# Kernel optimization log

Hardware: AMD Instinct MI355X
Metric: run time of the kernel (lower is better)

The kernel has to match this reference:

```python
import jax, jax.numpy as jnp
import numpy as np

EMBED_DIM = 512
NUM_HEADS = 8
HEAD_DIM = EMBED_DIM // NUM_HEADS
N = 4096
E = 131072
EPS = 1e-5
NEG = -1e9


def layer_norm(x, g, b):
    mu = jnp.mean(x, axis=-1, keepdims=True)
    var = jnp.mean(jnp.square(x - mu), axis=-1, keepdims=True)
    return (x - mu) * jax.lax.rsqrt(var + EPS) * g + b


def setup_inputs() -> dict:
    key = jax.random.key(0)
    ks = jax.random.split(key, 12)
    D = EMBED_DIM
    s = 1.0 / np.sqrt(D)
    return {
        "x": jax.random.normal(ks[0], (N, D), jnp.float32),
        "edge_index": jax.random.randint(ks[1], (2, E), 0, N, jnp.int64),
        "edge_weight": jax.random.uniform(ks[2], (E,), jnp.float32),
        "Wqkv": jax.random.normal(ks[3], (3 * D, D), jnp.float32) * s,
        "bqkv": jnp.zeros((3 * D,), jnp.float32),
        "Wo": jax.random.normal(ks[4], (D, D), jnp.float32) * s,
        "bo": jnp.zeros((D,), jnp.float32),
        "W1": jax.random.normal(ks[5], (D, D), jnp.float32) * s,
        "b1": jnp.zeros((D,), jnp.float32),
        "g1": jnp.ones((D,), jnp.float32),
        "beta1": jnp.zeros((D,), jnp.float32),
        "g2": jnp.ones((D,), jnp.float32),
        "beta2": jnp.zeros((D,), jnp.float32),
    }


def reference(x, edge_index, edge_weight, Wqkv, bqkv, Wo, bo, W1, b1, g1, beta1, g2, beta2):
    n = x.shape[0]
    # dense NxN additive bias: -1e9 everywhere, 0 on diagonal, edge weights at (dst, src)
    src, dst = edge_index[0], edge_index[1]
    diag = jnp.arange(n)
    bias = jnp.full((n, n), NEG, dtype=x.dtype)
    bias = bias.at[diag, diag].set(0.0)
    bias = bias.at[dst, src].set(edge_weight.astype(x.dtype))

    # multi-head self-attention (torch nn.MultiheadAttention semantics)
    qkv = x @ Wqkv.T + bqkv                       # (N, 3D)
    q, k, v = jnp.split(qkv, 3, axis=-1)          # each (N, D)
    q = q.reshape(n, NUM_HEADS, HEAD_DIM).transpose(1, 0, 2)  # (H, N, hd)
    k = k.reshape(n, NUM_HEADS, HEAD_DIM).transpose(1, 0, 2)
    v = v.reshape(n, NUM_HEADS, HEAD_DIM).transpose(1, 0, 2)
    scores = jnp.einsum("hnd,hmd->hnm", q, k) / np.sqrt(HEAD_DIM)  # (H, N, N)
    scores = scores + bias[None, :, :]
    attn = jax.nn.softmax(scores, axis=-1)
    out = jnp.einsum("hnm,hmd->hnd", attn, v)     # (H, N, hd)
    out = out.transpose(1, 0, 2).reshape(n, EMBED_DIM)
    attn_out = out @ Wo.T + bo

    # residual + LN + FFN (single linear, no activation) + residual + LN
    h = layer_norm(x + attn_out, g1, beta1)
    h = layer_norm(h + (h @ W1.T + b1), g2, beta2)
    return h
```

## Files before the change

### kernel.cpp

```cpp
#include <hip/hip_runtime.h>

#define NNODES 4096
#define DIM 512
#define QKVD 1536
#define MAXE 96

typedef __bf16 bf16_t;
typedef bf16_t bf16x8 __attribute__((ext_vector_type(8)));
typedef bf16_t bf16x2 __attribute__((ext_vector_type(2)));
typedef float f32x4 __attribute__((ext_vector_type(4)));
typedef unsigned int uint;

__global__ __launch_bounds__(256) void cast_all_k(const float* __restrict__ x,
                                                  const float* __restrict__ wqkv,
                                                  const float* __restrict__ wo,
                                                  const float* __restrict__ w1,
                                                  bf16_t* __restrict__ xb,
                                                  bf16_t* __restrict__ wqkvb,
                                                  bf16_t* __restrict__ wob,
                                                  bf16_t* __restrict__ w1b,
                                                  uint* __restrict__ deg) {
  int i = blockIdx.x * 256 + threadIdx.x;
  if (blockIdx.x < 16) deg[i] = 0u;
  const float* src;
  bf16_t* dst;
  int off;
  if (i < 524288) { src = x; dst = xb; off = i; }
  else if (i < 720896) { src = wqkv; dst = wqkvb; off = i - 524288; }
  else if (i < 786432) { src = wo; dst = wob; off = i - 720896; }
  else { src = w1; dst = w1b; off = i - 786432; }
  float4 v = ((const float4*)src)[off];
  dst[4 * off + 0] = (bf16_t)v.x;
  dst[4 * off + 1] = (bf16_t)v.y;
  dst[4 * off + 2] = (bf16_t)v.z;
  dst[4 * off + 3] = (bf16_t)v.w;
}

__global__ __launch_bounds__(256) void fill_bucket_k(const int* __restrict__ ei,
                                                     uint* __restrict__ deg,
                                                     int* __restrict__ colv,
                                                     uint* __restrict__ eidv, int E) {
  int e = blockIdx.x * 256 + threadIdx.x;
  if (e < E) {
    int src = ei[e] & (NNODES - 1);
    int dst = ei[E + e] & (NNODES - 1);
    uint pos = atomicAdd(&deg[dst], 1u);
    if (pos < MAXE) {
      colv[dst * MAXE + pos] = src;
      eidv[dst * MAXE + pos] = (uint)e + 1u;
    }
  }
}

template <bool OUT_BF16>
__global__ __launch_bounds__(256) void gemm_bt(const bf16_t* __restrict__ A,
                                               const bf16_t* __restrict__ B,
                                               const float* __restrict__ bias,
                                               void* __restrict__ Cout,
                                               int M, int Nt, int K) {
  __shared__ bf16_t As[128][40];
  __shared__ bf16_t Bs[64][40];
  const int t = threadIdx.x;
  const int lane = t & 63, w = t >> 6;
  const int wr = (w >> 1) * 64, wc = (w & 1) * 32;
  const int m0 = blockIdx.y * 128, n0 = blockIdx.x * 64;
  f32x4 acc[4][2] = {};
  const int r_ld = t >> 2;
  const int c_ld = (t & 3) * 8;

  for (int k0 = 0; k0 < K; k0 += 32) {
    *(int4*)&As[r_ld][c_ld] = *(const int4*)(A + (long)(m0 + r_ld) * K + k0 + c_ld);
    *(int4*)&As[r_ld + 64][c_ld] = *(const int4*)(A + (long)(m0 + r_ld + 64) * K + k0 + c_ld);
    *(int4*)&Bs[r_ld][c_ld] = *(const int4*)(B + (long)(n0 + r_ld) * K + k0 + c_ld);
    __syncthreads();
    bf16x8 af[4], bfr[2];
    const int kg = (lane >> 4) * 8;
#pragma unroll
    for (int i = 0; i < 4; ++i)
      af[i] = *(const bf16x8*)&As[wr + i * 16 + (lane & 15)][kg];
#pragma unroll
    for (int j = 0; j < 2; ++j)
      bfr[j] = *(const bf16x8*)&Bs[wc + j * 16 + (lane & 15)][kg];
#pragma unroll
    for (int i = 0; i < 4; ++i)
#pragma unroll
      for (int j = 0; j < 2; ++j)
        acc[i][j] = __builtin_amdgcn_mfma_f32_16x16x32_bf16(af[i], bfr[j], acc[i][j], 0, 0, 0);
    __syncthreads();
  }

  const int cr = (lane >> 4) * 4;
  const int cc = lane & 15;
#pragma unroll
  for (int i = 0; i < 4; ++i) {
#pragma unroll
    for (int j = 0; j < 2; ++j) {
      int n = n0 + wc + j * 16 + cc;
      float bv = bias[n];
#pragma unroll
      for (int r = 0; r < 4; ++r) {
        int m = m0 + wr + i * 16 + cr + r;
        float vv = acc[i][j][r] + bv;
        if (OUT_BF16)
          ((bf16_t*)Cout)[(long)m * Nt + n] = (bf16_t)vv;
        else
          ((float*)Cout)[(long)m * Nt + n] = vv;
      }
    }
  }
}

__global__ __launch_bounds__(256) void attn_fused_k(const bf16_t* __restrict__ qkv,
                                                    const float* __restrict__ ew,
                                                    const uint* __restrict__ deg,
                                                    const int* __restrict__ colv,
                                                    const uint* __restrict__ eidv,
                                                    bf16_t* __restrict__ outb) {
  __shared__ float sc[8][MAXE + 1];
  __shared__ int srcs[MAXE + 1];
  __shared__ uint eids[MAXE + 1];
  __shared__ int vld[MAXE + 1];
  __shared__ float invs_s[8];
  __shared__ float vacc[4][DIM];

  const int i = blockIdx.x;
  const int t = threadIdx.x;
  const int lane = t & 63, w = t >> 6;

  uint dg = deg[i];
  int L = (dg < (uint)MAXE) ? (int)dg : MAXE;
  int n = L + 1;

  if (t < L) {
    srcs[t] = colv[i * MAXE + t];
    eids[t] = eidv[i * MAXE + t];
  }
  if (t == L) { srcs[L] = i; eids[L] = 0u; }
  __syncthreads();

  if (t < n) {
    int sj = srcs[t];
    uint my = eids[t];
    int ok = 1;
    for (int j = 0; j < n; ++j)
      if (srcs[j] == sj && eids[j] > my) { ok = 0; break; }
    vld[t] = ok;
  }
  __syncthreads();

  const bf16x8 qv = *(const bf16x8*)(qkv + (long)i * QKVD + lane * 8);
  {
    int e = w;
    for (; e + 4 < n; e += 8) {
      int sa = srcs[e], sb = srcs[e + 4];
      const bf16x8 ka = *(const bf16x8*)(qkv + (long)sa * QKVD + DIM + lane * 8);
      const bf16x8 kb = *(const bf16x8*)(qkv + (long)sb * QKVD + DIM + lane * 8);
      float s0 = 0.f, s1 = 0.f;
#pragma unroll
      for (int j = 0; j < 8; ++j) {
        s0 += (float)qv[j] * (float)ka[j];
        s1 += (float)qv[j] * (float)kb[j];
      }
      s0 += __shfl_xor(s0, 1); s1 += __shfl_xor(s1, 1);
      s0 += __shfl_xor(s0, 2); s1 += __shfl_xor(s1, 2);
      s0 += __shfl_xor(s0, 4); s1 += __shfl_xor(s1, 4);
      if ((lane & 7) == 0) {
        int h = lane >> 3;
        float b0 = (eids[e] == 0u) ? 0.f : ew[eids[e] - 1u];
        float b1 = (eids[e + 4] == 0u) ? 0.f : ew[eids[e + 4] - 1u];
        sc[h][e] = vld[e] ? (s0 * 0.125f + b0) : -1e30f;
        sc[h][e + 4] = vld[e + 4] ? (s1 * 0.125f + b1) : -1e30f;
      }
    }
    if (e < n) {
      int sa = srcs[e];
      const bf16x8 ka = *(const bf16x8*)(qkv + (long)sa * QKVD + DIM + lane * 8);
      float s0 = 0.f;
#pragma unroll
      for (int j = 0; j < 8; ++j) s0 += (float)qv[j] * (float)ka[j];
      s0 += __shfl_xor(s0, 1);
      s0 += __shfl_xor(s0, 2);
      s0 += __shfl_xor(s0, 4);
      if ((lane & 7) == 0) {
        int h = lane >> 3;
        float b0 = (eids[e] == 0u) ? 0.f : ew[eids[e] - 1u];
        sc[h][e] = vld[e] ? (s0 * 0.125f + b0) : -1e30f;
      }
    }
  }
  __syncthreads();

#pragma unroll
  for (int hh = 0; hh < 2; ++hh) {
    int h = w * 2 + hh;
    float m = -1e30f;
    for (int e = lane; e < n; e += 64) m = fmaxf(m, sc[h][e]);
#pragma unroll
    for (int o = 32; o > 0; o >>= 1) m = fmaxf(m, __shfl_xor(m, o));
    float ps = 0.f;
    for (int e = lane; e < n; e += 64) {
      float ev = __expf(sc[h][e] - m);
      sc[h][e] = ev;
      ps += ev;
    }
#pragma unroll
    for (int o = 32; o > 0; o >>= 1) ps += __shfl_xor(ps, o);
    if (lane == 0) invs_s[h] = 1.f / ps;
  }
  __syncthreads();

  const int hl = lane >> 3;
  float a8[8] = {0.f, 0.f, 0.f, 0.f, 0.f, 0.f, 0.f, 0.f};
  {
    int e = w;
    for (; e + 4 < n; e += 8) {
      const bf16x8 v0 = *(const bf16x8*)(qkv + (long)srcs[e] * QKVD + 2 * DIM + lane * 8);
      const bf16x8 v1 = *(const bf16x8*)(qkv + (long)srcs[e + 4] * QKVD + 2 * DIM + lane * 8);
      float p0 = sc[hl][e], p1 = sc[hl][e + 4];
#pragma unroll
      for (int j = 0; j < 8; ++j) a8[j] += p0 * (float)v0[j] + p1 * (float)v1[j];
    }
    if (e < n) {
      const bf16x8 v0 = *(const bf16x8*)(qkv + (long)srcs[e] * QKVD + 2 * DIM + lane * 8);
      float p0 = sc[hl][e];
#pragma unroll
      for (int j = 0; j < 8; ++j) a8[j] += p0 * (float)v0[j];
    }
  }
#pragma unroll
  for (int j = 0; j < 8; ++j) vacc[w][lane * 8 + j] = a8[j];
  __syncthreads();

  {
    const int d0 = 2 * t;
    const int h = t >> 5;
    const float inv = invs_s[h];
    float s0 = vacc[0][d0] + vacc[1][d0] + vacc[2][d0] + vacc[3][d0];
    float s1 = vacc[0][d0 + 1] + vacc[1][d0 + 1] + vacc[2][d0 + 1] + vacc[3][d0 + 1];
    bf16x2 o2;
    o2[0] = (bf16_t)(s0 * inv);
    o2[1] = (bf16_t)(s1 * inv);
    *(bf16x2*)(outb + (long)i * DIM + d0) = o2;
  }
}

__global__ __launch_bounds__(64) void ln_k(const float* __restrict__ a,
                                           const float* __restrict__ b,
                                           const float* __restrict__ g,
                                           const float* __restrict__ beta,
                                           float* __restrict__ of,
                                           bf16_t* __restrict__ ob) {
  const int row = blockIdx.x;
  const int l = threadIdx.x;
  const float* pa = a + (long)row * DIM;
  const float* pb = b + (long)row * DIM;
  float v[8];
  float s = 0.f;
#pragma unroll
  for (int j = 0; j < 8; ++j) {
    int d = l + j * 64;
    v[j] = pa[d] + pb[d];
    s += v[j];
  }
#pragma unroll
  for (int o = 32; o > 0; o >>= 1) s += __shfl_xor(s, o);
  float mu = s * (1.f / 512.f);
  float q = 0.f;
#pragma unroll
  for (int j = 0; j < 8; ++j) {
    float dd = v[j] - mu;
    q += dd * dd;
  }
#pragma unroll
  for (int o = 32; o > 0; o >>= 1) q += __shfl_xor(q, o);
  float inv = rsqrtf(q * (1.f / 512.f) + 1e-5f);
#pragma unroll
  for (int j = 0; j < 8; ++j) {
    int d = l + j * 64;
    float y = (v[j] - mu) * inv * g[d] + beta[d];
    of[(long)row * DIM + d] = y;
    if (ob) ob[(long)row * DIM + d] = (bf16_t)y;
  }
}

extern "C" void kernel_launch(void* const* d_in, const int* in_sizes, int n_in,
                              void* d_out, int out_size, void* d_ws, size_t ws_size,
                              hipStream_t stream) {
  const float* x = (const float*)d_in[0];
  const int* ei = (const int*)d_in[1];
  const float* ew = (const float*)d_in[2];
  const float* Wqkv = (const float*)d_in[3];
  const float* bqkv = (const float*)d_in[4];
  const float* Wo = (const float*)d_in[5];
  const float* bo = (const float*)d_in[6];
  const float* W1 = (const float*)d_in[7];
  const float* b1 = (const float*)d_in[8];
  const float* g1 = (const float*)d_in[9];
  const float* be1 = (const float*)d_in[10];
  const float* g2 = (const float*)d_in[11];
  const float* be2 = (const float*)d_in[12];
  float* out = (float*)d_out;
  const int E = in_sizes[1] / 2;

  char* ws = (char*)d_ws;
  bf16_t* qkvb = (bf16_t*)(ws + 0);
  bf16_t* xb = (bf16_t*)(ws + 12582912);
  bf16_t* Wqkvb = (bf16_t*)(ws + 16777216);
  bf16_t* Wob = (bf16_t*)(ws + 18350080);
  bf16_t* W1b = (bf16_t*)(ws + 18874368);
  bf16_t* outb = (bf16_t*)(ws + 19398656);
  float* h = (float*)(ws + 23592960);
  bf16_t* hb = (bf16_t*)(ws + 31981568);
  float* f = (float*)(ws + 36175872);
  uint* deg = (uint*)(ws + 23592960);
  int* colv = (int*)(ws + 23609344);
  uint* eidv = (uint*)(ws + 25182208);
  float* attn_out = (float*)(ws + 0);

  cast_all_k<<<3328, 256, 0, stream>>>(x, Wqkv, Wo, W1, xb, Wqkvb, Wob, W1b, deg);
  fill_bucket_k<<<(E + 255) / 256, 256, 0, stream>>>(ei, deg, colv, eidv, E);

  gemm_bt<true><<<dim3(QKVD / 64, NNODES / 128), 256, 0, stream>>>(
      xb, Wqkvb, bqkv, (void*)qkvb, NNODES, QKVD, DIM);

  attn_fused_k<<<NNODES, 256, 0, stream>>>(qkvb, ew, deg, colv, eidv, outb);

  gemm_bt<false><<<dim3(DIM / 64, NNODES / 128), 256, 0, stream>>>(
      outb, Wob, bo, (void*)attn_out, NNODES, DIM, DIM);

  ln_k<<<NNODES, 64, 0, stream>>>(x, attn_out, g1, be1, h, hb);

  gemm_bt<false><<<dim3(DIM / 64, NNODES / 128), 256, 0, stream>>>(
      hb, W1b, b1, (void*)f, NNODES, DIM, DIM);

  ln_k<<<NNODES, 64, 0, stream>>>(h, f, g2, be2, out, nullptr);
}
```

Before: 119.2 us.

## Fuse output and FFN GEMMs with residual LayerNorm; unroll attention edge loops

Replaces the Wo and W1 GEMMs plus separate LayerNorm kernels with a fused GEMM+residual+LN kernel. Each block computes full 512-wide rows for 16 nodes, staging B in LDS with register prefetch, and computes the row statistics in the epilogue using the sum and sum-of-squares form. This removes two launches and the fp32 intermediate round-trips to global memory. In exchange, every block rereads all of B for only 16 rows, giving 256 blocks, and the single-pass variance can lose precision. The attention kernel's K and V gather loops are also unrolled from 2 to 4 edges per iteration to raise memory-level parallelism.

```diff
diff --git a/kernel.cpp b/kernel.cpp
--- a/kernel.cpp
+++ b/kernel.cpp
@@ -52,11 +52,10 @@
   }
 }
 
-template <bool OUT_BF16>
 __global__ __launch_bounds__(256) void gemm_bt(const bf16_t* __restrict__ A,
                                                const bf16_t* __restrict__ B,
                                                const float* __restrict__ bias,
-                                               void* __restrict__ Cout,
+                                               bf16_t* __restrict__ Cout,
                                                int M, int Nt, int K) {
   __shared__ bf16_t As[128][40];
   __shared__ bf16_t Bs[64][40];
@@ -100,12 +99,108 @@
 #pragma unroll
       for (int r = 0; r < 4; ++r) {
         int m = m0 + wr + i * 16 + cr + r;
-        float vv = acc[i][j][r] + bv;
-        if (OUT_BF16)
-          ((bf16_t*)Cout)[(long)m * Nt + n] = (bf16_t)vv;
-        else
-          ((float*)Cout)[(long)m * Nt + n] = vv;
-      }
+        Cout[(long)m * Nt + n] = (bf16_t)(acc[i][j][r] + bv);
+      }
+    }
+  }
+}
+
+template <bool OUT_BF16>
+__global__ __launch_bounds__(256) void gemm_ln_k(const bf16_t* __restrict__ A,
+                                                 const bf16_t* __restrict__ B,
+                                                 const float* __restrict__ bias,
+                                                 const float* __restrict__ res,
+                                                 const float* __restrict__ g,
+                                                 const float* __restrict__ beta,
+                                                 float* __restrict__ outf,
+                                                 bf16_t* __restrict__ outbb) {
+  __shared__ bf16_t Bs[512][40];
+  __shared__ float rs[4][16], rq[4][16];
+  const int t = threadIdx.x;
+  const int lane = t & 63, w = t >> 6;
+  const int m0 = blockIdx.x * 16;
+  const int cc = lane & 15;
+  const int rg = lane >> 4;
+
+  f32x4 acc[8] = {};
+  const int brow = t >> 2;
+  const int bcol = (t & 3) * 8;
+
+  int4 breg[8];
+#pragma unroll
+  for (int c = 0; c < 8; ++c)
+    breg[c] = *(const int4*)(B + (long)(brow + c * 64) * 512 + bcol);
+
+  for (int k0 = 0; k0 < 512; k0 += 32) {
+#pragma unroll
+    for (int c = 0; c < 8; ++c)
+      *(int4*)&Bs[brow + c * 64][bcol] = breg[c];
+    __syncthreads();
+    if (k0 + 32 < 512) {
+#pragma unroll
+      for (int c = 0; c < 8; ++c)
+        breg[c] = *(const int4*)(B + (long)(brow + c * 64) * 512 + (k0 + 32) + bcol);
+    }
+    const bf16x8 af = *(const bf16x8*)(A + (long)(m0 + cc) * 512 + k0 + rg * 8);
+    const int kg = rg * 8;
+#pragma unroll
+    for (int j = 0; j < 8; ++j) {
+      const bf16x8 bf = *(const bf16x8*)&Bs[w * 128 + j * 16 + cc][kg];
+      acc[j] = __builtin_amdgcn_mfma_f32_16x16x32_bf16(af, bf, acc[j], 0, 0, 0);
+    }
+    __syncthreads();
+  }
+
+  float ps[4] = {0.f, 0.f, 0.f, 0.f}, pq[4] = {0.f, 0.f, 0.f, 0.f};
+#pragma unroll
+  for (int j = 0; j < 8; ++j) {
+    int n = w * 128 + j * 16 + cc;
+    float bv = bias[n];
+#pragma unroll
+    for (int r = 0; r < 4; ++r) {
+      int m = m0 + rg * 4 + r;
+      float v = acc[j][r] + bv + res[(long)m * 512 + n];
+      acc[j][r] = v;
+      ps[r] += v;
+      pq[r] += v * v;
+    }
+  }
+#pragma unroll
+  for (int o = 1; o < 16; o <<= 1) {
+#pragma unroll
+    for (int r = 0; r < 4; ++r) {
+      ps[r] += __shfl_xor(ps[r], o);
+      pq[r] += __shfl_xor(pq[r], o);
+    }
+  }
+  if (cc == 0) {
+#pragma unroll
+    for (int r = 0; r < 4; ++r) {
+      rs[w][rg * 4 + r] = ps[r];
+      rq[w][rg * 4 + r] = pq[r];
+    }
+  }
+  __syncthreads();
+  float mu[4], inv[4];
+#pragma unroll
+  for (int r = 0; r < 4; ++r) {
+    int m = rg * 4 + r;
+    float s = rs[0][m] + rs[1][m] + rs[2][m] + rs[3][m];
+    float q = rq[0][m] + rq[1][m] + rq[2][m] + rq[3][m];
+    float mm = s * (1.f / 512.f);
+    mu[r] = mm;
+    inv[r] = rsqrtf(q * (1.f / 512.f) - mm * mm + 1e-5f);
+  }
+#pragma unroll
+  for (int j = 0; j < 8; ++j) {
+    int n = w * 128 + j * 16 + cc;
+    float gv = g[n], bev = beta[n];
+#pragma unroll
+    for (int r = 0; r < 4; ++r) {
+      int m = m0 + rg * 4 + r;
+      float y = (acc[j][r] - mu[r]) * inv[r] * gv + bev;
+      outf[(long)m * 512 + n] = y;
+      if (OUT_BF16) outbb[(long)m * 512 + n] = (bf16_t)y;
     }
   }
 }
@@ -116,7 +211,7 @@
                                                     const int* __restrict__ colv,
                                                     const uint* __restrict__ eidv,
                                                     bf16_t* __restrict__ outb) {
-  __shared__ float sc[8][MAXE + 1];
+  __shared__ float scs[8][MAXE + 1];
   __shared__ int srcs[MAXE + 1];
   __shared__ uint eids[MAXE + 1];
   __shared__ int vld[MAXE + 1];
@@ -151,40 +246,45 @@
   const bf16x8 qv = *(const bf16x8*)(qkv + (long)i * QKVD + lane * 8);
   {
     int e = w;
-    for (; e + 4 < n; e += 8) {
-      int sa = srcs[e], sb = srcs[e + 4];
-      const bf16x8 ka = *(const bf16x8*)(qkv + (long)sa * QKVD + DIM + lane * 8);
-      const bf16x8 kb = *(const bf16x8*)(qkv + (long)sb * QKVD + DIM + lane * 8);
-      float s0 = 0.f, s1 = 0.f;
+    for (; e + 12 < n; e += 16) {
+      const bf16x8 ka = *(const bf16x8*)(qkv + (long)srcs[e] * QKVD + DIM + lane * 8);
+      const bf16x8 kb = *(const bf16x8*)(qkv + (long)srcs[e + 4] * QKVD + DIM + lane * 8);
+      const bf16x8 kc = *(const bf16x8*)(qkv + (long)srcs[e + 8] * QKVD + DIM + lane * 8);
+      const bf16x8 kd = *(const bf16x8*)(qkv + (long)srcs[e + 12] * QKVD + DIM + lane * 8);
+      float d0 = 0.f, d1 = 0.f, d2 = 0.f, d3 = 0.f;
 #pragma unroll
       for (int j = 0; j < 8; ++j) {
-        s0 += (float)qv[j] * (float)ka[j];
-        s1 += (float)qv[j] * (float)kb[j];
-      }
-      s0 += __shfl_xor(s0, 1); s1 += __shfl_xor(s1, 1);
-      s0 += __shfl_xor(s0, 2); s1 += __shfl_xor(s1, 2);
-      s0 += __shfl_xor(s0, 4); s1 += __shfl_xor(s1, 4);
+        float q = (float)qv[j];
+        d0 += q * (float)ka[j];
+        d1 += q * (float)kb[j];
+        d2 += q * (float)kc[j];
+        d3 += q * (float)kd[j];
+      }
+#pragma unroll
+      for (int o = 1; o < 8; o <<= 1) {
+        d0 += __shfl_xor(d0, o);
+        d1 += __shfl_xor(d1, o);
+        d2 += __shfl_xor(d2, o);
+        d3 += __shfl_xor(d3, o);
+      }
       if ((lane & 7) == 0) {
         int h = lane >> 3;
-        float b0 = (eids[e] == 0u) ? 0.f : ew[eids[e] - 1u];
-        float b1 = (eids[e + 4] == 0u) ? 0.f : ew[eids[e + 4] - 1u];
-        sc[h][e] = vld[e] ? (s0 * 0.125f + b0) : -1e30f;
-        sc[h][e + 4] = vld[e + 4] ? (s1 * 0.125f + b1) : -1e30f;
-      }
-    }
-    if (e < n) {
-      int sa = srcs[e];
-      const bf16x8 ka = *(const bf16x8*)(qkv + (long)sa * QKVD + DIM + lane * 8);
-      float s0 = 0.f;
-#pragma unroll
-      for (int j = 0; j < 8; ++j) s0 += (float)qv[j] * (float)ka[j];
-      s0 += __shfl_xor(s0, 1);
-      s0 += __shfl_xor(s0, 2);
-      s0 += __shfl_xor(s0, 4);
+        scs[h][e] = vld[e] ? (d0 * 0.125f + ((eids[e] == 0u) ? 0.f : ew[eids[e] - 1u])) : -1e30f;
+        scs[h][e + 4] = vld[e + 4] ? (d1 * 0.125f + ((eids[e + 4] == 0u) ? 0.f : ew[eids[e + 4] - 1u])) : -1e30f;
+        scs[h][e + 8] = vld[e + 8] ? (d2 * 0.125f + ((eids[e + 8] == 0u) ? 0.f : ew[eids[e + 8] - 1u])) : -1e30f;
+        scs[h][e + 12] = vld[e + 12] ? (d3 * 0.125f + ((eids[e + 12] == 0u) ? 0.f : ew[eids[e + 12] - 1u])) : -1e30f;
+      }
+    }
+    for (; e < n; e += 4) {
+      const bf16x8 ka = *(const bf16x8*)(qkv + (long)srcs[e] * QKVD + DIM + lane * 8);
+      float d0 = 0.f;
+#pragma unroll
+      for (int j = 0; j < 8; ++j) d0 += (float)qv[j] * (float)ka[j];
+#pragma unroll
+      for (int o = 1; o < 8; o <<= 1) d0 += __shfl_xor(d0, o);
       if ((lane & 7) == 0) {
         int h = lane >> 3;
-        float b0 = (eids[e] == 0u) ? 0.f : ew[eids[e] - 1u];
-        sc[h][e] = vld[e] ? (s0 * 0.125f + b0) : -1e30f;
+        scs[h][e] = vld[e] ? (d0 * 0.125f + ((eids[e] == 0u) ? 0.f : ew[eids[e] - 1u])) : -1e30f;
       }
     }
   }
@@ -194,13 +294,13 @@
   for (int hh = 0; hh < 2; ++hh) {
     int h = w * 2 + hh;
     float m = -1e30f;
-    for (int e = lane; e < n; e += 64) m = fmaxf(m, sc[h][e]);
+    for (int e = lane; e < n; e += 64) m = fmaxf(m, scs[h][e]);
 #pragma unroll
     for (int o = 32; o > 0; o >>= 1) m = fmaxf(m, __shfl_xor(m, o));
     float ps = 0.f;
     for (int e = lane; e < n; e += 64) {
-      float ev = __expf(sc[h][e] - m);
-      sc[h][e] = ev;
+      float ev = __expf(scs[h][e] - m);
+      scs[h][e] = ev;
       ps += ev;
     }
 #pragma unroll
@@ -213,16 +313,19 @@
   float a8[8] = {0.f, 0.f, 0.f, 0.f, 0.f, 0.f, 0.f, 0.f};
   {
     int e = w;
-    for (; e + 4 < n; e += 8) {
+    for (; e + 12 < n; e += 16) {
       const bf16x8 v0 = *(const bf16x8*)(qkv + (long)srcs[e] * QKVD + 2 * DIM + lane * 8);
       const bf16x8 v1 = *(const bf16x8*)(qkv + (long)srcs[e + 4] * QKVD + 2 * DIM + lane * 8);
-      float p0 = sc[hl][e], p1 = sc[hl][e + 4];
-#pragma unroll
-      for (int j = 0; j < 8; ++j) a8[j] += p0 * (float)v0[j] + p1 * (float)v1[j];
-    }
-    if (e < n) {
+      const bf16x8 v2 = *(const bf16x8*)(qkv + (long)srcs[e + 8] * QKVD + 2 * DIM + lane * 8);
+      const bf16x8 v3 = *(const bf16x8*)(qkv + (long)srcs[e + 12] * QKVD + 2 * DIM + lane * 8);
+      float p0 = scs[hl][e], p1 = scs[hl][e + 4], p2 = scs[hl][e + 8], p3 = scs[hl][e + 12];
+#pragma unroll
+      for (int j = 0; j < 8; ++j)
+        a8[j] += p0 * (float)v0[j] + p1 * (float)v1[j] + p2 * (float)v2[j] + p3 * (float)v3[j];
+    }
+    for (; e < n; e += 4) {
       const bf16x8 v0 = *(const bf16x8*)(qkv + (long)srcs[e] * QKVD + 2 * DIM + lane * 8);
-      float p0 = sc[hl][e];
+      float p0 = scs[hl][e];
 #pragma unroll
       for (int j = 0; j < 8; ++j) a8[j] += p0 * (float)v0[j];
     }
@@ -241,45 +344,6 @@
     o2[0] = (bf16_t)(s0 * inv);
     o2[1] = (bf16_t)(s1 * inv);
     *(bf16x2*)(outb + (long)i * DIM + d0) = o2;
-  }
-}
-
-__global__ __launch_bounds__(64) void ln_k(const float* __restrict__ a,
-                                           const float* __restrict__ b,
-                                           const float* __restrict__ g,
-                                           const float* __restrict__ beta,
-                                           float* __restrict__ of,
-                                           bf16_t* __restrict__ ob) {
-  const int row = blockIdx.x;
-  const int l = threadIdx.x;
-  const float* pa = a + (long)row * DIM;
-  const float* pb = b + (long)row * DIM;
-  float v[8];
-  float s = 0.f;
-#pragma unroll
-  for (int j = 0; j < 8; ++j) {
-    int d = l + j * 64;
-    v[j] = pa[d] + pb[d];
-    s += v[j];
-  }
-#pragma unroll
-  for (int o = 32; o > 0; o >>= 1) s += __shfl_xor(s, o);
-  float mu = s * (1.f / 512.f);
-  float q = 0.f;
-#pragma unroll
-  for (int j = 0; j < 8; ++j) {
-    float dd = v[j] - mu;
-    q += dd * dd;
-  }
-#pragma unroll
-  for (int o = 32; o > 0; o >>= 1) q += __shfl_xor(q, o);
-  float inv = rsqrtf(q * (1.f / 512.f) + 1e-5f);
-#pragma unroll
-  for (int j = 0; j < 8; ++j) {
-    int d = l + j * 64;
-    float y = (v[j] - mu) * inv * g[d] + beta[d];
-    of[(long)row * DIM + d] = y;
-    if (ob) ob[(long)row * DIM + d] = (bf16_t)y;
   }
 }
 
@@ -311,27 +375,19 @@
   bf16_t* outb = (bf16_t*)(ws + 19398656);
   float* h = (float*)(ws + 23592960);
   bf16_t* hb = (bf16_t*)(ws + 31981568);
-  float* f = (float*)(ws + 36175872);
   uint* deg = (uint*)(ws + 23592960);
   int* colv = (int*)(ws + 23609344);
   uint* eidv = (uint*)(ws + 25182208);
-  float* attn_out = (float*)(ws + 0);
 
   cast_all_k<<<3328, 256, 0, stream>>>(x, Wqkv, Wo, W1, xb, Wqkvb, Wob, W1b, deg);
   fill_bucket_k<<<(E + 255) / 256, 256, 0, stream>>>(ei, deg, colv, eidv, E);
 
-  gemm_bt<true><<<dim3(QKVD / 64, NNODES / 128), 256, 0, stream>>>(
-      xb, Wqkvb, bqkv, (void*)qkvb, NNODES, QKVD, DIM);
+  gemm_bt<<<dim3(QKVD / 64, NNODES / 128), 256, 0, stream>>>(
+      xb, Wqkvb, bqkv, qkvb, NNODES, QKVD, DIM);
 
   attn_fused_k<<<NNODES, 256, 0, stream>>>(qkvb, ew, deg, colv, eidv, outb);
 
-  gemm_bt<false><<<dim3(DIM / 64, NNODES / 128), 256, 0, stream>>>(
-      outb, Wob, bo, (void*)attn_out, NNODES, DIM, DIM);
-
-  ln_k<<<NNODES, 64, 0, stream>>>(x, attn_out, g1, be1, h, hb);
-
-  gemm_bt<false><<<dim3(DIM / 64, NNODES / 128), 256, 0, stream>>>(
-      hb, W1b, b1, (void*)f, NNODES, DIM, DIM);
-
-  ln_k<<<NNODES, 64, 0, stream>>>(h, f, g2, be2, out, nullptr);
-}
+  gemm_ln_k<true><<<NNODES / 16, 256, 0, stream>>>(outb, Wob, bo, x, g1, be1, h, hb);
+
+  gemm_ln_k<false><<<NNODES / 16, 256, 0, stream>>>(hb, W1b, b1, h, g2, be2, out, nullptr);
+}
```

Measured after the change: 177.5 us. 1.49x slower.

## Fuse edge bucketing into a larger-tile QKV GEMM launch

Applied to the files above, without the earlier changes.

Merges the edge-bucket fill kernel into the QKV projection kernel, with extra blocks past index 384 doing the atomic bucket fill while the first 384 blocks compute the GEMM. The GEMM tile grows from 128x64 to 128x128 with a 4x4 MFMA accumulator per wave, and the duplicate-edge check becomes a branchless loop. This removes one launch and lets the scatter overlap the GEMM, at the cost of more registers per GEMM block and fewer GEMM blocks.

```diff
diff --git a/kernel.cpp b/kernel.cpp
--- a/kernel.cpp
+++ b/kernel.cpp
@@ -36,18 +36,76 @@
   dst[4 * off + 3] = (bf16_t)v.w;
 }
 
-__global__ __launch_bounds__(256) void fill_bucket_k(const int* __restrict__ ei,
-                                                     uint* __restrict__ deg,
-                                                     int* __restrict__ colv,
-                                                     uint* __restrict__ eidv, int E) {
-  int e = blockIdx.x * 256 + threadIdx.x;
-  if (e < E) {
-    int src = ei[e] & (NNODES - 1);
-    int dst = ei[E + e] & (NNODES - 1);
-    uint pos = atomicAdd(&deg[dst], 1u);
-    if (pos < MAXE) {
-      colv[dst * MAXE + pos] = src;
-      eidv[dst * MAXE + pos] = (uint)e + 1u;
+__global__ __launch_bounds__(256) void qkv_fill_k(const bf16_t* __restrict__ A,
+                                                  const bf16_t* __restrict__ B,
+                                                  const float* __restrict__ bias,
+                                                  bf16_t* __restrict__ Cout,
+                                                  const int* __restrict__ ei,
+                                                  uint* __restrict__ deg,
+                                                  int* __restrict__ colv,
+                                                  uint* __restrict__ eidv, int E) {
+  __shared__ bf16_t As[128][40];
+  __shared__ bf16_t Bs[128][40];
+  const int bid = blockIdx.x;
+  const int t = threadIdx.x;
+
+  if (bid >= 384) {
+    int e = (bid - 384) * 256 + t;
+    if (e < E) {
+      int src = ei[e] & (NNODES - 1);
+      int dst = ei[E + e] & (NNODES - 1);
+      uint pos = atomicAdd(&deg[dst], 1u);
+      if (pos < MAXE) {
+        colv[dst * MAXE + pos] = src;
+        eidv[dst * MAXE + pos] = (uint)e + 1u;
+      }
+    }
+    return;
+  }
+
+  const int lane = t & 63, w = t >> 6;
+  const int wr = (w >> 1) * 64, wc = (w & 1) * 64;
+  const int m0 = (bid / 12) * 128, n0 = (bid % 12) * 128;
+  f32x4 acc[4][4] = {};
+  const int r_ld = t >> 2;
+  const int c_ld = (t & 3) * 8;
+
+  for (int k0 = 0; k0 < 512; k0 += 32) {
+#pragma unroll
+    for (int seg = 0; seg < 2; ++seg) {
+      int row = r_ld + seg * 64;
+      *(int4*)&As[row][c_ld] = *(const int4*)(A + (long)(m0 + row) * 512 + k0 + c_ld);
+      *(int4*)&Bs[row][c_ld] = *(const int4*)(B + (long)(n0 + row) * 512 + k0 + c_ld);
+    }
+    __syncthreads();
+    bf16x8 af[4], bfr[4];
+    const int kg = (lane >> 4) * 8;
+#pragma unroll
+    for (int i = 0; i < 4; ++i) {
+      af[i] = *(const bf16x8*)&As[wr + i * 16 + (lane & 15)][kg];
+      bfr[i] = *(const bf16x8*)&Bs[wc + i * 16 + (lane & 15)][kg];
+    }
+#pragma unroll
+    for (int i = 0; i < 4; ++i)
+#pragma unroll
+      for (int j = 0; j < 4; ++j)
+        acc[i][j] = __builtin_amdgcn_mfma_f32_16x16x32_bf16(af[i], bfr[j], acc[i][j], 0, 0, 0);
+    __syncthreads();
+  }
+
+  const int cr = (lane >> 4) * 4;
+  const int cc = lane & 15;
+#pragma unroll
+  for (int i = 0; i < 4; ++i) {
+#pragma unroll
+    for (int j = 0; j < 4; ++j) {
+      int n = n0 + wc + j * 16 + cc;
+      float bv = bias[n];
+#pragma unroll
+      for (int r = 0; r < 4; ++r) {
+        int m = m0 + wr + i * 16 + cr + r;
+        Cout[(long)m * QKVD + n] = (bf16_t)(acc[i][j][r] + bv);
+      }
     }
   }
 }
@@ -116,7 +174,7 @@
                                                     const int* __restrict__ colv,
                                                     const uint* __restrict__ eidv,
                                                     bf16_t* __restrict__ outb) {
-  __shared__ float sc[8][MAXE + 1];
+  __shared__ float scs[8][MAXE + 1];
   __shared__ int srcs[MAXE + 1];
   __shared__ uint eids[MAXE + 1];
   __shared__ int vld[MAXE + 1];
@@ -143,7 +201,7 @@
     uint my = eids[t];
     int ok = 1;
     for (int j = 0; j < n; ++j)
-      if (srcs[j] == sj && eids[j] > my) { ok = 0; break; }
+      ok &= !((srcs[j] == sj) & (eids[j] > my));
     vld[t] = ok;
   }
   __syncthreads();
@@ -168,8 +226,8 @@
         int h = lane >> 3;
         float b0 = (eids[e] == 0u) ? 0.f : ew[eids[e] - 1u];
         float b1 = (eids[e + 4] == 0u) ? 0.f : ew[eids[e + 4] - 1u];
-        sc[h][e] = vld[e] ? (s0 * 0.125f + b0) : -1e30f;
-        sc[h][e + 4] = vld[e + 4] ? (s1 * 0.125f + b1) : -1e30f;
+        scs[h][e] = vld[e] ? (s0 * 0.125f + b0) : -1e30f;
+        scs[h][e + 4] = vld[e + 4] ? (s1 * 0.125f + b1) : -1e30f;
       }
     }
     if (e < n) {
@@ -184,7 +242,7 @@
       if ((lane & 7) == 0) {
         int h = lane >> 3;
         float b0 = (eids[e] == 0u) ? 0.f : ew[eids[e] - 1u];
-        sc[h][e] = vld[e] ? (s0 * 0.125f + b0) : -1e30f;
+        scs[h][e] = vld[e] ? (s0 * 0.125f + b0) : -1e30f;
       }
     }
   }
@@ -194,13 +252,13 @@
   for (int hh = 0; hh < 2; ++hh) {
     int h = w * 2 + hh;
     float m = -1e30f;
-    for (int e = lane; e < n; e += 64) m = fmaxf(m, sc[h][e]);
+    for (int e = lane; e < n; e += 64) m = fmaxf(m, scs[h][e]);
 #pragma unroll
     for (int o = 32; o > 0; o >>= 1) m = fmaxf(m, __shfl_xor(m, o));
     float ps = 0.f;
     for (int e = lane; e < n; e += 64) {
-      float ev = __expf(sc[h][e] - m);
-      sc[h][e] = ev;
+      float ev = __expf(scs[h][e] - m);
+      scs[h][e] = ev;
       ps += ev;
     }
 #pragma unroll
@@ -216,13 +274,13 @@
     for (; e + 4 < n; e += 8) {
       const bf16x8 v0 = *(const bf16x8*)(qkv + (long)srcs[e] * QKVD + 2 * DIM + lane * 8);
       const bf16x8 v1 = *(const bf16x8*)(qkv + (long)srcs[e + 4] * QKVD + 2 * DIM + lane * 8);
-      float p0 = sc[hl][e], p1 = sc[hl][e + 4];
+      float p0 = scs[hl][e], p1 = scs[hl][e + 4];
 #pragma unroll
       for (int j = 0; j < 8; ++j) a8[j] += p0 * (float)v0[j] + p1 * (float)v1[j];
     }
     if (e < n) {
       const bf16x8 v0 = *(const bf16x8*)(qkv + (long)srcs[e] * QKVD + 2 * DIM + lane * 8);
-      float p0 = sc[hl][e];
+      float p0 = scs[hl][e];
 #pragma unroll
       for (int j = 0; j < 8; ++j) a8[j] += p0 * (float)v0[j];
     }
@@ -318,10 +376,9 @@
   float* attn_out = (float*)(ws + 0);
 
   cast_all_k<<<3328, 256, 0, stream>>>(x, Wqkv, Wo, W1, xb, Wqkvb, Wob, W1b, deg);
-  fill_bucket_k<<<(E + 255) / 256, 256, 0, stream>>>(ei, deg, colv, eidv, E);
-
-  gemm_bt<true><<<dim3(QKVD / 64, NNODES / 128), 256, 0, stream>>>(
-      xb, Wqkvb, bqkv, (void*)qkvb, NNODES, QKVD, DIM);
+
+  qkv_fill_k<<<384 + (E + 255) / 256, 256, 0, stream>>>(
+      xb, Wqkvb, bqkv, qkvb, ei, deg, colv, eidv, E);
 
   attn_fused_k<<<NNODES, 256, 0, stream>>>(qkvb, ew, deg, colv, eidv, outb);
 
```

Measured after the change: 107.0 us, median of 2. 1.11x faster.
